# Optimization experiments

Measured on AMD Instinct MI355X. Metric: run time of the kernel, lower is better.

Reference implementation:

```python
import jax, jax.numpy as jnp
import numpy as np

B, T, D = 2, 512, 1024
H = 16
DH = D // H          # 64 head dim
E = 8                # experts
K = 2                # top-k routing
F = 4 * D            # expert hidden dim


def _layernorm(x, s, b, eps=1e-5):
    mu = jnp.mean(x, axis=-1, keepdims=True)
    var = jnp.var(x, axis=-1, keepdims=True)
    return (x - mu) * jax.lax.rsqrt(var + eps) * s + b


def setup_inputs() -> dict:
    key = jax.random.key(0)
    ks = jax.random.split(key, 16)
    sd = 0.02
    return {
        "x": jax.random.normal(ks[0], (B, T, D), jnp.float32),
        "text_state": jax.random.normal(ks[1], (B, D), jnp.float32),
        "ln1_s": jnp.ones((D,), jnp.float32),
        "ln1_b": jnp.zeros((D,), jnp.float32),
        "w_qkv": jax.random.normal(ks[2], (D, 3 * D), jnp.float32) * sd,
        "b_qkv": jnp.zeros((3 * D,), jnp.float32),
        "w_o": jax.random.normal(ks[3], (D, D), jnp.float32) * sd,
        "b_o": jnp.zeros((D,), jnp.float32),
        "rel_bias": jax.random.normal(ks[4], (H, 2 * T - 1), jnp.float32) * sd,
        "ln2_s": jnp.ones((D,), jnp.float32),
        "ln2_b": jnp.zeros((D,), jnp.float32),
        "w_txt": jax.random.normal(ks[5], (D, D), jnp.float32) * sd,
        "b_txt": jnp.zeros((D,), jnp.float32),
        "w_r": jax.random.normal(ks[6], (D, E), jnp.float32) * sd,
        "b_r": jnp.zeros((E,), jnp.float32),
        "w1": jax.random.normal(ks[7], (E, D, F), jnp.float32) * sd,
        "b1": jnp.zeros((E, F), jnp.float32),
        "w2": jax.random.normal(ks[8], (E, F, D), jnp.float32) * sd,
        "b2": jnp.zeros((E, D), jnp.float32),
    }


def reference(x, text_state, ln1_s, ln1_b, w_qkv, b_qkv, w_o, b_o, rel_bias,
              ln2_s, ln2_b, w_txt, b_txt, w_r, b_r, w1, b1, w2, b2):
    # ---- temporal-bias multi-head self-attention (pre-LN, residual) ----
    h = _layernorm(x, ln1_s, ln1_b)
    qkv = (h @ w_qkv + b_qkv).reshape(B, T, 3, H, DH)
    q, k, v = qkv[:, :, 0], qkv[:, :, 1], qkv[:, :, 2]       # [B,T,H,DH]
    scores = jnp.einsum("bthd,bshd->bhts", q, k) / np.sqrt(DH).astype(np.float32)
    idx = jnp.arange(T)
    rel = idx[None, :] - idx[:, None] + (T - 1)              # [T,T] in [0, 2T-2]
    scores = scores + rel_bias[:, rel][None]                 # broadcast [1,H,T,T]
    attn = jax.nn.softmax(scores, axis=-1)
    ctx = jnp.einsum("bhts,bshd->bthd", attn, v).reshape(B, T, D)
    x = x + ctx @ w_o + b_o

    # ---- top-k MoE feed-forward with text-conditioned router ----
    h2 = _layernorm(x, ln2_s, ln2_b)
    router_in = h2 + (text_state @ w_txt + b_txt)[:, None, :]
    probs = jax.nn.softmax(router_in @ w_r + b_r, axis=-1)   # [B,T,E]
    topv, topi = jax.lax.top_k(probs, K)                     # [B,T,K]
    gates = topv / jnp.sum(topv, axis=-1, keepdims=True)
    gates_full = jnp.einsum("btk,btke->bte", gates, jax.nn.one_hot(topi, E, dtype=x.dtype))
    # dense grouped-expert compute, sparsely combined (same math as dispatch)
    hid = jax.nn.gelu(jnp.einsum("btd,edf->btef", h2, w1) + b1)      # [B,T,E,F]
    eout = jnp.einsum("btef,efd->bted", hid, w2) + b2                # [B,T,E,D]
    y = jnp.einsum("bte,bted->btd", gates_full, eout)
    x = x + y

    diag = jnp.mean(probs, axis=(0, 1))                      # expert load [E]
    return x, diag
```

## Files before the change

kernel.cpp:

```cpp
#include <hip/hip_runtime.h>
#include <hip/hip_bf16.h>
#include <math.h>

#define BB 2
#define TT 512
#define DD 1024
#define HH 16
#define DHH 64
#define EE 8
#define FF 4096
#define NTOK 1024
#define CAP 2560

typedef __attribute__((ext_vector_type(4))) float f32x4;
typedef __attribute__((ext_vector_type(8))) short short8;

__device__ __forceinline__ short f2b(float f) {
    __hip_bfloat16 h = __float2bfloat16(f);
    return *reinterpret_cast<short*>(&h);
}

__device__ __forceinline__ void gload16(const short* g, short* l) {
    __builtin_amdgcn_global_load_lds((const __attribute__((address_space(1))) unsigned int*)g,
                                     (__attribute__((address_space(3))) unsigned int*)l,
                                     16, 0, 0);
}

template <int BF>
__global__ __launch_bounds__(256) void ln_kernel(const float* __restrict__ x,
                                                 const float* __restrict__ s,
                                                 const float* __restrict__ b,
                                                 void* __restrict__ outp) {
    int row = blockIdx.x;
    int tid = threadIdx.x;
    const float* xr = x + (size_t)row * DD;
    float sm = 0.f, sq = 0.f;
    for (int i = tid; i < DD; i += 256) {
        float v = xr[i];
        sm += v; sq += v * v;
    }
    #pragma unroll
    for (int o = 32; o; o >>= 1) {
        sm += __shfl_down(sm, o);
        sq += __shfl_down(sq, o);
    }
    __shared__ float r1[4], r2[4];
    if ((tid & 63) == 0) { r1[tid >> 6] = sm; r2[tid >> 6] = sq; }
    __syncthreads();
    float tot  = r1[0] + r1[1] + r1[2] + r1[3];
    float totq = r2[0] + r2[1] + r2[2] + r2[3];
    float mu  = tot * (1.f / DD);
    float var = totq * (1.f / DD) - mu * mu;
    float inv = rsqrtf(var + 1e-5f);
    for (int i = tid; i < DD; i += 256) {
        float v = (xr[i] - mu) * inv * s[i] + b[i];
        if (BF) ((short*)outp)[(size_t)row * DD + i] = f2b(v);
        else    ((float*)outp)[(size_t)row * DD + i] = v;
    }
}

__global__ __launch_bounds__(256) void transpose_cast(const float* __restrict__ src,
                                                      short* __restrict__ dst,
                                                      int K, int N) {
    __shared__ float t[32][33];
    src += (size_t)blockIdx.z * K * N;
    dst += (size_t)blockIdx.z * K * N;
    int k0 = blockIdx.y * 32, n0 = blockIdx.x * 32;
    int tx = threadIdx.x & 31, ty = threadIdx.x >> 5;
    #pragma unroll
    for (int p = 0; p < 4; p++) {
        int k = k0 + ty + p * 8;
        t[ty + p * 8][tx] = src[(size_t)k * N + n0 + tx];
    }
    __syncthreads();
    #pragma unroll
    for (int p = 0; p < 4; p++) {
        int n = n0 + ty + p * 8;
        dst[(size_t)n * K + k0 + tx] = f2b(t[tx][ty + p * 8]);
    }
}

__global__ __launch_bounds__(256) void v_transpose(const short* __restrict__ Vb,
                                                   short* __restrict__ VTb) {
    __shared__ short t[32][33];
    int bh = blockIdx.z;
    const short* src = Vb + (size_t)bh * TT * DHH;
    short* dst = VTb + (size_t)bh * DHH * TT;
    int t0 = blockIdx.x * 32, d0 = blockIdx.y * 32;
    int tx = threadIdx.x & 31, ty = threadIdx.x >> 5;
    #pragma unroll
    for (int p = 0; p < 4; p++)
        t[ty + p * 8][tx] = src[(size_t)(t0 + ty + p * 8) * DHH + d0 + tx];
    __syncthreads();
    #pragma unroll
    for (int p = 0; p < 4; p++)
        dst[(size_t)(d0 + ty + p * 8) * TT + t0 + tx] = t[tx][ty + p * 8];
}

__device__ __forceinline__ void gemm_loop(const short* __restrict__ A,
                                          const short* __restrict__ B,
                                          int K, short* As, short* Bs,
                                          f32x4 acc[2][2], int m0, int n0, int tid) {
    int wave = tid >> 6, lane = tid & 63;
    int wr = wave >> 1, wc = wave & 1;
    int lrow = lane & 15, lk = lane >> 4;
    int sr = tid >> 3, ss = tid & 7;
    int sswz = (ss ^ (sr & 7)) * 8;
    const short* Ag0 = A + (size_t)(m0 + sr) * K + sswz;
    const short* Ag1 = A + (size_t)(m0 + sr + 32) * K + sswz;
    const short* Bg0 = B + (size_t)(n0 + sr) * K + sswz;
    const short* Bg1 = B + (size_t)(n0 + sr + 32) * K + sswz;
    short* lA0 = As + wave * 512;
    short* lA1 = As + 2048 + wave * 512;
    short* lB0 = Bs + wave * 512;
    short* lB1 = Bs + 2048 + wave * 512;
    for (int k0 = 0; k0 < K; k0 += 64) {
        gload16(Ag0 + k0, lA0);
        gload16(Ag1 + k0, lA1);
        gload16(Bg0 + k0, lB0);
        gload16(Bg1 + k0, lB1);
        __syncthreads();
        #pragma unroll
        for (int kk = 0; kk < 2; kk++) {
            int slot = kk * 4 + lk;
            short8 a[2], b[2];
            #pragma unroll
            for (int i = 0; i < 2; i++) {
                int row = wr * 32 + i * 16 + lrow;
                uint4 v = ((const uint4*)As)[row * 8 + (slot ^ (row & 7))];
                a[i] = *(short8*)&v;
            }
            #pragma unroll
            for (int j = 0; j < 2; j++) {
                int row = wc * 32 + j * 16 + lrow;
                uint4 v = ((const uint4*)Bs)[row * 8 + (slot ^ (row & 7))];
                b[j] = *(short8*)&v;
            }
            #pragma unroll
            for (int i = 0; i < 2; i++)
                #pragma unroll
                for (int j = 0; j < 2; j++)
                    acc[i][j] = __builtin_amdgcn_mfma_f32_16x16x32_bf16(a[i], b[j], acc[i][j], 0, 0, 0);
        }
        __syncthreads();
    }
}

template <int MODE>
__global__ __launch_bounds__(256) void gemm_mfma(const short* __restrict__ A,
                                                 const short* __restrict__ Bw,
                                                 const float* __restrict__ bias,
                                                 const float* __restrict__ res,
                                                 float* __restrict__ C,
                                                 int N, int K) {
    __shared__ short As[4096];
    __shared__ short Bs[4096];
    int tid = threadIdx.x;
    int m0 = blockIdx.y * 64, n0 = blockIdx.x * 64;
    f32x4 acc[2][2] = {};
    gemm_loop(A, Bw, K, As, Bs, acc, m0, n0, tid);
    int wave = tid >> 6, lane = tid & 63;
    int wr = wave >> 1, wc = wave & 1;
    int lrow = lane & 15, lk = lane >> 4;
    #pragma unroll
    for (int i = 0; i < 2; i++) {
        #pragma unroll
        for (int j = 0; j < 2; j++) {
            int col = n0 + wc * 32 + j * 16 + lrow;
            float bv = bias[col];
            #pragma unroll
            for (int r = 0; r < 4; r++) {
                int row = m0 + wr * 32 + i * 16 + lk * 4 + r;
                float v = acc[i][j][r] + bv;
                if (MODE == 1) v += res[(size_t)row * N + col];
                C[(size_t)row * N + col] = v;
            }
        }
    }
}

__global__ __launch_bounds__(256) void qkv_mfma(const short* __restrict__ A,
                                                const short* __restrict__ Bw,
                                                const float* __restrict__ bias,
                                                short* __restrict__ Qb,
                                                short* __restrict__ Kb,
                                                short* __restrict__ Vb) {
    __shared__ short As[4096];
    __shared__ short Bs[4096];
    int tid = threadIdx.x;
    int m0 = blockIdx.y * 64, n0 = blockIdx.x * 64;
    f32x4 acc[2][2] = {};
    gemm_loop(A, Bw, DD, As, Bs, acc, m0, n0, tid);
    int wave = tid >> 6, lane = tid & 63;
    int wr = wave >> 1, wc = wave & 1;
    int lrow = lane & 15, lk = lane >> 4;
    int part = n0 >> 10;
    int h = (n0 & 1023) >> 6;
    short* dst = (part == 0) ? Qb : ((part == 1) ? Kb : Vb);
    #pragma unroll
    for (int i = 0; i < 2; i++) {
        #pragma unroll
        for (int j = 0; j < 2; j++) {
            int d = wc * 32 + j * 16 + lrow;
            float bv = bias[n0 + d];
            #pragma unroll
            for (int r = 0; r < 4; r++) {
                int row = m0 + wr * 32 + i * 16 + lk * 4 + r;
                int b = row >> 9, t = row & (TT - 1);
                dst[(((size_t)(b * HH + h)) * TT + t) * DHH + d] = f2b(acc[i][j][r] + bv);
            }
        }
    }
}

__global__ __launch_bounds__(256) void scores_mfma(const short* __restrict__ Qb,
                                                   const short* __restrict__ Kb,
                                                   float* __restrict__ S) {
    __shared__ short As[4096];
    __shared__ short Bs[4096];
    int tid = threadIdx.x;
    int bh = blockIdx.z;
    const short* A = Qb + (size_t)bh * TT * DHH;
    const short* B = Kb + (size_t)bh * TT * DHH;
    float* Sp = S + (size_t)bh * TT * TT;
    int m0 = blockIdx.y * 64, n0 = blockIdx.x * 64;
    f32x4 acc[2][2] = {};
    gemm_loop(A, B, DHH, As, Bs, acc, m0, n0, tid);
    int wave = tid >> 6, lane = tid & 63;
    int wr = wave >> 1, wc = wave & 1;
    int lrow = lane & 15, lk = lane >> 4;
    #pragma unroll
    for (int i = 0; i < 2; i++)
        #pragma unroll
        for (int j = 0; j < 2; j++) {
            int col = n0 + wc * 32 + j * 16 + lrow;
            #pragma unroll
            for (int r = 0; r < 4; r++) {
                int row = m0 + wr * 32 + i * 16 + lk * 4 + r;
                Sp[(size_t)row * TT + col] = acc[i][j][r];
            }
        }
}

__global__ __launch_bounds__(256) void softmax_kernel(const float* __restrict__ S,
                                                      const float* __restrict__ rel_bias,
                                                      short* __restrict__ P) {
    int row = blockIdx.x * 4 + (threadIdx.x >> 6);
    int lane = threadIdx.x & 63;
    int t = row & (TT - 1), h = (row >> 9) & (HH - 1);
    const float* Sr = S + (size_t)row * TT;
    const float* br = rel_bias + h * (2 * TT - 1) + (TT - 1) - t;
    float v[8];
    float mx = -1e30f;
    #pragma unroll
    for (int i = 0; i < 8; i++) {
        int s = lane + i * 64;
        v[i] = Sr[s] * 0.125f + br[s];
        mx = fmaxf(mx, v[i]);
    }
    #pragma unroll
    for (int o = 32; o; o >>= 1) mx = fmaxf(mx, __shfl_xor(mx, o));
    float sum = 0.f;
    #pragma unroll
    for (int i = 0; i < 8; i++) { v[i] = expf(v[i] - mx); sum += v[i]; }
    #pragma unroll
    for (int o = 32; o; o >>= 1) sum += __shfl_xor(sum, o);
    float inv = 1.f / sum;
    #pragma unroll
    for (int i = 0; i < 8; i++)
        P[(size_t)row * TT + lane + i * 64] = f2b(v[i] * inv);
}

__global__ __launch_bounds__(256) void pv_mfma(const short* __restrict__ P,
                                               const short* __restrict__ VTb,
                                               short* __restrict__ ctxb) {
    __shared__ short As[4096];
    __shared__ short Bs[4096];
    int tid = threadIdx.x;
    int bh = blockIdx.z;
    int h = bh & (HH - 1), b = bh >> 4;
    const short* A = P + (size_t)bh * TT * TT;
    const short* B = VTb + (size_t)bh * DHH * TT;
    int m0 = blockIdx.y * 64;
    f32x4 acc[2][2] = {};
    gemm_loop(A, B, TT, As, Bs, acc, m0, 0, tid);
    int wave = tid >> 6, lane = tid & 63;
    int wr = wave >> 1, wc = wave & 1;
    int lrow = lane & 15, lk = lane >> 4;
    #pragma unroll
    for (int i = 0; i < 2; i++)
        #pragma unroll
        for (int j = 0; j < 2; j++) {
            int d = wc * 32 + j * 16 + lrow;
            #pragma unroll
            for (int r = 0; r < 4; r++) {
                int row = m0 + wr * 32 + i * 16 + lk * 4 + r;
                ctxb[((size_t)(b * TT + row)) * DD + h * DHH + d] = f2b(acc[i][j][r]);
            }
        }
}

__global__ __launch_bounds__(256) void moe_gemm1_mfma(const short* __restrict__ Ag,
                                                      const short* __restrict__ W1t,
                                                      const float* __restrict__ b1,
                                                      const int* __restrict__ counts,
                                                      const int* __restrict__ offs,
                                                      short* __restrict__ hid) {
    int e = blockIdx.y >> 4, tile = blockIdx.y & 15;
    int cnt = counts[e];
    int pcnt = (cnt + 63) & ~63;
    int row0 = tile * 64;
    if (row0 >= pcnt) return;
    int base = offs[e];
    const short* A  = Ag + (size_t)base * DD;
    const short* Bw = W1t + (size_t)e * FF * DD;
    __shared__ short As[4096];
    __shared__ short Bs[4096];
    int tid = threadIdx.x;
    int n0 = blockIdx.x * 64;
    f32x4 acc[2][2] = {};
    gemm_loop(A, Bw, DD, As, Bs, acc, row0, n0, tid);
    int wave = tid >> 6, lane = tid & 63;
    int wr = wave >> 1, wc = wave & 1;
    int lrow = lane & 15, lk = lane >> 4;
    #pragma unroll
    for (int i = 0; i < 2; i++) {
        #pragma unroll
        for (int j = 0; j < 2; j++) {
            int col = n0 + wc * 32 + j * 16 + lrow;
            float bv = b1[e * FF + col];
            #pragma unroll
            for (int r = 0; r < 4; r++) {
                int row = row0 + wr * 32 + i * 16 + lk * 4 + r;
                float v = acc[i][j][r] + bv;
                float u = 0.7978845608028654f * (v + 0.044715f * v * v * v);
                float g = 0.5f * v * (1.f + tanhf(u));
                hid[(size_t)(base + row) * FF + col] = f2b(g);
            }
        }
    }
}

__global__ __launch_bounds__(256) void moe_gemm2_mfma(const short* __restrict__ hid,
                                                      const short* __restrict__ W2t,
                                                      const float* __restrict__ b2,
                                                      const float* __restrict__ pair_gate,
                                                      const int* __restrict__ counts,
                                                      const int* __restrict__ offs,
                                                      float* __restrict__ pair_out) {
    int e = blockIdx.y >> 4, tile = blockIdx.y & 15;
    int cnt = counts[e];
    int pcnt = (cnt + 63) & ~63;
    int row0 = tile * 64;
    if (row0 >= pcnt) return;
    int base = offs[e];
    const short* A  = hid + (size_t)base * FF;
    const short* Bw = W2t + (size_t)e * DD * FF;
    __shared__ short As[4096];
    __shared__ short Bs[4096];
    int tid = threadIdx.x;
    int n0 = blockIdx.x * 64;
    f32x4 acc[2][2] = {};
    gemm_loop(A, Bw, FF, As, Bs, acc, row0, n0, tid);
    int wave = tid >> 6, lane = tid & 63;
    int wr = wave >> 1, wc = wave & 1;
    int lrow = lane & 15, lk = lane >> 4;
    #pragma unroll
    for (int i = 0; i < 2; i++) {
        #pragma unroll
        for (int j = 0; j < 2; j++) {
            int col = n0 + wc * 32 + j * 16 + lrow;
            float bv = b2[e * DD + col];
            #pragma unroll
            for (int r = 0; r < 4; r++) {
                int row = row0 + wr * 32 + i * 16 + lk * 4 + r;
                float g = pair_gate[base + row];
                pair_out[(size_t)(base + row) * DD + col] = g * (acc[i][j][r] + bv);
            }
        }
    }
}

__global__ __launch_bounds__(256) void txt_kernel(const float* __restrict__ ts,
                                                  const float* __restrict__ w,
                                                  const float* __restrict__ bias,
                                                  float* __restrict__ out) {
    int gid = blockIdx.x * 256 + threadIdx.x;
    int b = gid >> 10;
    int n = gid & (DD - 1);
    float acc = 0.f;
    for (int d = 0; d < DD; d++) acc += ts[b * DD + d] * w[(size_t)d * DD + n];
    out[gid] = acc + bias[n];
}

__global__ __launch_bounds__(256) void router_kernel(const float* __restrict__ h2,
                                                     const float* __restrict__ txt,
                                                     const float* __restrict__ w_r,
                                                     const float* __restrict__ b_r,
                                                     float* __restrict__ probs,
                                                     float* __restrict__ gates,
                                                     int* __restrict__ counts) {
    int row = blockIdx.x;
    int b = row >> 9;
    int tid = threadIdx.x;
    float acc[EE] = {};
    for (int d = tid; d < DD; d += 256) {
        float r = h2[(size_t)row * DD + d] + txt[b * DD + d];
        #pragma unroll
        for (int e = 0; e < EE; e++) acc[e] += r * w_r[d * EE + e];
    }
    #pragma unroll
    for (int e = 0; e < EE; e++)
        #pragma unroll
        for (int o = 32; o; o >>= 1) acc[e] += __shfl_down(acc[e], o);
    __shared__ float lds[4][EE];
    int lane = tid & 63, w = tid >> 6;
    if (lane == 0)
        for (int e = 0; e < EE; e++) lds[w][e] = acc[e];
    __syncthreads();
    if (tid == 0) {
        float lg[EE], p[EE];
        float mx = -1e30f;
        for (int e = 0; e < EE; e++) {
            lg[e] = lds[0][e] + lds[1][e] + lds[2][e] + lds[3][e] + b_r[e];
            mx = fmaxf(mx, lg[e]);
        }
        float sum = 0.f;
        for (int e = 0; e < EE; e++) { p[e] = expf(lg[e] - mx); sum += p[e]; }
        float invs = 1.f / sum;
        for (int e = 0; e < EE; e++) { p[e] *= invs; probs[row * EE + e] = p[e]; }
        int i1 = 0;
        for (int e = 1; e < EE; e++) if (p[e] > p[i1]) i1 = e;
        int i2 = (i1 == 0) ? 1 : 0;
        for (int e = 0; e < EE; e++) if (e != i1 && p[e] > p[i2]) i2 = e;
        float gs = p[i1] + p[i2];
        for (int e = 0; e < EE; e++) gates[row * EE + e] = 0.f;
        gates[row * EE + i1] = p[i1] / gs;
        gates[row * EE + i2] = p[i2] / gs;
        atomicAdd(&counts[i1], 1);
        atomicAdd(&counts[i2], 1);
    }
}

__global__ void offs_kernel(const int* __restrict__ counts, int* __restrict__ offs) {
    if (threadIdx.x == 0) {
        int acc = 0;
        for (int e = 0; e < EE; e++) { offs[e] = acc; acc += (counts[e] + 63) & ~63; }
    }
}

__global__ __launch_bounds__(256) void scatter_kernel(const float* __restrict__ gates,
                                                      const int* __restrict__ offs,
                                                      int* __restrict__ fill,
                                                      int* __restrict__ tok_pos,
                                                      float* __restrict__ pair_gate) {
    int t = blockIdx.x * 256 + threadIdx.x;
    if (t >= NTOK) return;
    int slot = 0;
    for (int e = 0; e < EE; e++) {
        float g = gates[t * EE + e];
        if (g > 0.f) {
            int pos = offs[e] + atomicAdd(&fill[e], 1);
            tok_pos[t * 2 + slot] = pos;
            pair_gate[pos] = g;
            slot++;
        }
    }
}

__global__ __launch_bounds__(256) void gather_tokens(const float* __restrict__ h2,
                                                     const int* __restrict__ tok_pos,
                                                     short* __restrict__ Ag) {
    int i = blockIdx.x;
    int pos = tok_pos[i];
    int t = i >> 1;
    int d = threadIdx.x * 4;
    #pragma unroll
    for (int k = 0; k < 4; k++)
        Ag[(size_t)pos * DD + d + k] = f2b(h2[(size_t)t * DD + d + k]);
}

__global__ __launch_bounds__(256) void diag_kernel(const float* __restrict__ probs,
                                                   float* __restrict__ out) {
    int e = blockIdx.x;
    int tid = threadIdx.x;
    float s = 0.f;
    for (int t = tid; t < NTOK; t += 256) s += probs[t * EE + e];
    #pragma unroll
    for (int o = 32; o; o >>= 1) s += __shfl_down(s, o);
    __shared__ float red[4];
    if ((tid & 63) == 0) red[tid >> 6] = s;
    __syncthreads();
    if (tid == 0) out[e] = (red[0] + red[1] + red[2] + red[3]) * (1.f / NTOK);
}

__global__ __launch_bounds__(256) void finaladd_kernel(float* __restrict__ out,
                                                       const float* __restrict__ pair_out,
                                                       const int* __restrict__ tok_pos) {
    int t = blockIdx.x;
    int pA = tok_pos[2 * t], pB = tok_pos[2 * t + 1];
    int d = threadIdx.x * 4;
    float4 a = *(const float4*)&out[(size_t)t * DD + d];
    float4 u = *(const float4*)&pair_out[(size_t)pA * DD + d];
    float4 v = *(const float4*)&pair_out[(size_t)pB * DD + d];
    a.x += u.x + v.x; a.y += u.y + v.y; a.z += u.z + v.z; a.w += u.w + v.w;
    *(float4*)&out[(size_t)t * DD + d] = a;
}

extern "C" void kernel_launch(void* const* d_in, const int* in_sizes, int n_in,
                              void* d_out, int out_size, void* d_ws, size_t ws_size,
                              hipStream_t stream) {
    const float* x          = (const float*)d_in[0];
    const float* text_state = (const float*)d_in[1];
    const float* ln1_s      = (const float*)d_in[2];
    const float* ln1_b      = (const float*)d_in[3];
    const float* w_qkv      = (const float*)d_in[4];
    const float* b_qkv      = (const float*)d_in[5];
    const float* w_o        = (const float*)d_in[6];
    const float* b_o        = (const float*)d_in[7];
    const float* rel_bias   = (const float*)d_in[8];
    const float* ln2_s      = (const float*)d_in[9];
    const float* ln2_b      = (const float*)d_in[10];
    const float* w_txt      = (const float*)d_in[11];
    const float* b_txt      = (const float*)d_in[12];
    const float* w_r        = (const float*)d_in[13];
    const float* b_r        = (const float*)d_in[14];
    const float* w1         = (const float*)d_in[15];
    const float* b1         = (const float*)d_in[16];
    const float* w2         = (const float*)d_in[17];
    const float* b2         = (const float*)d_in[18];

    float* out = (float*)d_out;

    char* p = (char*)d_ws;
    auto alloc = [&](size_t bytes) { char* r = p; p += (bytes + 255) & ~(size_t)255; return r; };
    short* h1b      = (short*)alloc((size_t)NTOK * DD * 2);
    short* Qb       = (short*)alloc((size_t)NTOK * DD * 2);
    short* Kb       = (short*)alloc((size_t)NTOK * DD * 2);
    short* Vb       = (short*)alloc((size_t)NTOK * DD * 2);
    short* VTb      = (short*)alloc((size_t)NTOK * DD * 2);
    char*  region1  = alloc((size_t)BB * HH * TT * TT * 4);
    char*  region2  = alloc((size_t)BB * HH * TT * TT * 2);
    short* ctxb     = (short*)alloc((size_t)NTOK * DD * 2);
    float* h2       = (float*)alloc((size_t)NTOK * DD * 4);
    float* txt      = (float*)alloc((size_t)BB * DD * 4);
    float* probs    = (float*)alloc((size_t)NTOK * EE * 4);
    float* gates    = (float*)alloc((size_t)NTOK * EE * 4);
    float* pair_gate= (float*)alloc((size_t)CAP * 4);
    int*   counts   = (int*)alloc(8 * 4);
    int*   fill     = (int*)alloc(8 * 4);
    int*   offs     = (int*)alloc(8 * 4);
    int*   tok_pos  = (int*)alloc((size_t)NTOK * 2 * 4);
    short* wqkvT    = (short*)alloc((size_t)3 * DD * DD * 2);
    short* woT      = (short*)alloc((size_t)DD * DD * 2);
    short* w1T      = (short*)alloc((size_t)EE * FF * DD * 2);
    short* w2T      = (short*)alloc((size_t)EE * DD * FF * 2);

    float* S        = (float*)region1;
    short* P        = (short*)region2;
    short* Ag       = (short*)region1;
    short* hid      = (short*)(region1 + ((size_t)CAP * DD * 2 + 255 & ~(size_t)255));
    float* pair_out = (float*)region2;

    transpose_cast<<<dim3(3 * DD / 32, DD / 32, 1), 256, 0, stream>>>(w_qkv, wqkvT, DD, 3 * DD);
    transpose_cast<<<dim3(DD / 32, DD / 32, 1), 256, 0, stream>>>(w_o, woT, DD, DD);
    transpose_cast<<<dim3(FF / 32, DD / 32, EE), 256, 0, stream>>>(w1, w1T, DD, FF);
    transpose_cast<<<dim3(DD / 32, FF / 32, EE), 256, 0, stream>>>(w2, w2T, FF, DD);

    ln_kernel<1><<<NTOK, 256, 0, stream>>>(x, ln1_s, ln1_b, h1b);
    qkv_mfma<<<dim3(3 * DD / 64, NTOK / 64), 256, 0, stream>>>(h1b, wqkvT, b_qkv, Qb, Kb, Vb);
    v_transpose<<<dim3(TT / 32, DHH / 32, BB * HH), 256, 0, stream>>>(Vb, VTb);
    scores_mfma<<<dim3(TT / 64, TT / 64, BB * HH), 256, 0, stream>>>(Qb, Kb, S);
    softmax_kernel<<<BB * HH * TT / 4, 256, 0, stream>>>(S, rel_bias, P);
    pv_mfma<<<dim3(1, TT / 64, BB * HH), 256, 0, stream>>>(P, VTb, ctxb);
    gemm_mfma<1><<<dim3(DD / 64, NTOK / 64), 256, 0, stream>>>(ctxb, woT, b_o, x, out, DD, DD);
    ln_kernel<0><<<NTOK, 256, 0, stream>>>(out, ln2_s, ln2_b, h2);
    txt_kernel<<<(BB * DD) / 256, 256, 0, stream>>>(text_state, w_txt, b_txt, txt);
    hipMemsetAsync(counts, 0, 8 * 4, stream);
    hipMemsetAsync(fill, 0, 8 * 4, stream);
    hipMemsetAsync(Ag, 0, (size_t)CAP * DD * 2, stream);
    router_kernel<<<NTOK, 256, 0, stream>>>(h2, txt, w_r, b_r, probs, gates, counts);
    offs_kernel<<<1, 64, 0, stream>>>(counts, offs);
    scatter_kernel<<<NTOK / 256, 256, 0, stream>>>(gates, offs, fill, tok_pos, pair_gate);
    gather_tokens<<<NTOK * 2, 256, 0, stream>>>(h2, tok_pos, Ag);
    diag_kernel<<<EE, 256, 0, stream>>>(probs, out + (size_t)NTOK * DD);
    moe_gemm1_mfma<<<dim3(FF / 64, EE * 16), 256, 0, stream>>>(Ag, w1T, b1, counts, offs, hid);
    moe_gemm2_mfma<<<dim3(DD / 64, EE * 16), 256, 0, stream>>>(hid, w2T, b2, pair_gate, counts, offs, pair_out);
    finaladd_kernel<<<NTOK, 256, 0, stream>>>(out, pair_out, tok_pos);
}
```

Measured before the change: 415.2 us.

## Widen MFMA GEMM tiles to 64x128 and vectorize the weight transpose-cast

Adds a wider GEMM main loop in which each block computes a 64x128 output tile. Each wave now holds 2x4 MFMA accumulators, so A-tile reuse doubles and the number of blocks halves. The QKV, scores, output-projection and both MoE GEMMs use it; the PV GEMM keeps the 64-wide loop. The weight transpose-cast moves to 64x64 tiles with float4 loads and short4 stores to cut memory transactions. The MoE grid also doubles its per-expert tile slots, which adds blocks that exit early, and the larger LDS and register footprint may lower occupancy.

```diff
diff --git a/kernel.cpp b/kernel.cpp
--- a/kernel.cpp
+++ b/kernel.cpp
@@ -62,21 +62,28 @@
 __global__ __launch_bounds__(256) void transpose_cast(const float* __restrict__ src,
                                                       short* __restrict__ dst,
                                                       int K, int N) {
-    __shared__ float t[32][33];
+    __shared__ float t[64][65];
     src += (size_t)blockIdx.z * K * N;
     dst += (size_t)blockIdx.z * K * N;
-    int k0 = blockIdx.y * 32, n0 = blockIdx.x * 32;
-    int tx = threadIdx.x & 31, ty = threadIdx.x >> 5;
+    int k0 = blockIdx.y * 64, n0 = blockIdx.x * 64;
+    int rr = threadIdx.x >> 4;
+    int cc = (threadIdx.x & 15) * 4;
     #pragma unroll
     for (int p = 0; p < 4; p++) {
-        int k = k0 + ty + p * 8;
-        t[ty + p * 8][tx] = src[(size_t)k * N + n0 + tx];
+        float4 v = *(const float4*)&src[(size_t)(k0 + rr + p * 16) * N + n0 + cc];
+        t[rr + p * 16][cc]     = v.x;
+        t[rr + p * 16][cc + 1] = v.y;
+        t[rr + p * 16][cc + 2] = v.z;
+        t[rr + p * 16][cc + 3] = v.w;
     }
     __syncthreads();
     #pragma unroll
     for (int p = 0; p < 4; p++) {
-        int n = n0 + ty + p * 8;
-        dst[(size_t)n * K + k0 + tx] = f2b(t[tx][ty + p * 8]);
+        int n = rr + p * 16;
+        short4 o;
+        o.x = f2b(t[cc][n]); o.y = f2b(t[cc + 1][n]);
+        o.z = f2b(t[cc + 2][n]); o.w = f2b(t[cc + 3][n]);
+        *(short4*)&dst[(size_t)(n0 + n) * K + k0 + cc] = o;
     }
 }
 
@@ -97,10 +104,65 @@
         dst[(size_t)(d0 + ty + p * 8) * TT + t0 + tx] = t[tx][ty + p * 8];
 }
 
-__device__ __forceinline__ void gemm_loop(const short* __restrict__ A,
-                                          const short* __restrict__ B,
-                                          int K, short* As, short* Bs,
-                                          f32x4 acc[2][2], int m0, int n0, int tid) {
+__device__ __forceinline__ void gemm_loop_w(const short* __restrict__ A,
+                                            const short* __restrict__ B,
+                                            int K, short* As, short* Bs,
+                                            f32x4 acc[2][4], int m0, int n0, int tid) {
+    int wave = tid >> 6, lane = tid & 63;
+    int wr = wave >> 1, wc = wave & 1;
+    int lrow = lane & 15, lk = lane >> 4;
+    int sr = tid >> 3, ss = tid & 7;
+    int sswz = (ss ^ (sr & 7)) * 8;
+    const short* Ag0 = A + (size_t)(m0 + sr) * K + sswz;
+    const short* Ag1 = A + (size_t)(m0 + sr + 32) * K + sswz;
+    const short* Bg0 = B + (size_t)(n0 + sr) * K + sswz;
+    const short* Bg1 = B + (size_t)(n0 + sr + 32) * K + sswz;
+    const short* Bg2 = B + (size_t)(n0 + sr + 64) * K + sswz;
+    const short* Bg3 = B + (size_t)(n0 + sr + 96) * K + sswz;
+    short* lA0 = As + wave * 512;
+    short* lA1 = As + 2048 + wave * 512;
+    short* lB0 = Bs + wave * 512;
+    short* lB1 = Bs + 2048 + wave * 512;
+    short* lB2 = Bs + 4096 + wave * 512;
+    short* lB3 = Bs + 6144 + wave * 512;
+    for (int k0 = 0; k0 < K; k0 += 64) {
+        gload16(Ag0 + k0, lA0);
+        gload16(Ag1 + k0, lA1);
+        gload16(Bg0 + k0, lB0);
+        gload16(Bg1 + k0, lB1);
+        gload16(Bg2 + k0, lB2);
+        gload16(Bg3 + k0, lB3);
+        __syncthreads();
+        #pragma unroll
+        for (int kk = 0; kk < 2; kk++) {
+            int slot = kk * 4 + lk;
+            short8 a[2], b[4];
+            #pragma unroll
+            for (int i = 0; i < 2; i++) {
+                int row = wr * 32 + i * 16 + lrow;
+                uint4 v = ((const uint4*)As)[row * 8 + (slot ^ (row & 7))];
+                a[i] = *(short8*)&v;
+            }
+            #pragma unroll
+            for (int j = 0; j < 4; j++) {
+                int row = wc * 64 + j * 16 + lrow;
+                uint4 v = ((const uint4*)Bs)[row * 8 + (slot ^ (row & 7))];
+                b[j] = *(short8*)&v;
+            }
+            #pragma unroll
+            for (int i = 0; i < 2; i++)
+                #pragma unroll
+                for (int j = 0; j < 4; j++)
+                    acc[i][j] = __builtin_amdgcn_mfma_f32_16x16x32_bf16(a[i], b[j], acc[i][j], 0, 0, 0);
+        }
+        __syncthreads();
+    }
+}
+
+__device__ __forceinline__ void gemm_loop64(const short* __restrict__ A,
+                                            const short* __restrict__ B,
+                                            int K, short* As, short* Bs,
+                                            f32x4 acc[2][2], int m0, int n0, int tid) {
     int wave = tid >> 6, lane = tid & 63;
     int wr = wave >> 1, wc = wave & 1;
     int lrow = lane & 15, lk = lane >> 4;
@@ -154,19 +216,19 @@
                                                  float* __restrict__ C,
                                                  int N, int K) {
     __shared__ short As[4096];
-    __shared__ short Bs[4096];
-    int tid = threadIdx.x;
-    int m0 = blockIdx.y * 64, n0 = blockIdx.x * 64;
-    f32x4 acc[2][2] = {};
-    gemm_loop(A, Bw, K, As, Bs, acc, m0, n0, tid);
+    __shared__ short Bs[8192];
+    int tid = threadIdx.x;
+    int m0 = blockIdx.y * 64, n0 = blockIdx.x * 128;
+    f32x4 acc[2][4] = {};
+    gemm_loop_w(A, Bw, K, As, Bs, acc, m0, n0, tid);
     int wave = tid >> 6, lane = tid & 63;
     int wr = wave >> 1, wc = wave & 1;
     int lrow = lane & 15, lk = lane >> 4;
     #pragma unroll
     for (int i = 0; i < 2; i++) {
         #pragma unroll
-        for (int j = 0; j < 2; j++) {
-            int col = n0 + wc * 32 + j * 16 + lrow;
+        for (int j = 0; j < 4; j++) {
+            int col = n0 + wc * 64 + j * 16 + lrow;
             float bv = bias[col];
             #pragma unroll
             for (int r = 0; r < 4; r++) {
@@ -186,23 +248,24 @@
                                                 short* __restrict__ Kb,
                                                 short* __restrict__ Vb) {
     __shared__ short As[4096];
-    __shared__ short Bs[4096];
-    int tid = threadIdx.x;
-    int m0 = blockIdx.y * 64, n0 = blockIdx.x * 64;
-    f32x4 acc[2][2] = {};
-    gemm_loop(A, Bw, DD, As, Bs, acc, m0, n0, tid);
-    int wave = tid >> 6, lane = tid & 63;
-    int wr = wave >> 1, wc = wave & 1;
-    int lrow = lane & 15, lk = lane >> 4;
-    int part = n0 >> 10;
-    int h = (n0 & 1023) >> 6;
-    short* dst = (part == 0) ? Qb : ((part == 1) ? Kb : Vb);
+    __shared__ short Bs[8192];
+    int tid = threadIdx.x;
+    int m0 = blockIdx.y * 64, n0 = blockIdx.x * 128;
+    f32x4 acc[2][4] = {};
+    gemm_loop_w(A, Bw, DD, As, Bs, acc, m0, n0, tid);
+    int wave = tid >> 6, lane = tid & 63;
+    int wr = wave >> 1, wc = wave & 1;
+    int lrow = lane & 15, lk = lane >> 4;
     #pragma unroll
     for (int i = 0; i < 2; i++) {
         #pragma unroll
-        for (int j = 0; j < 2; j++) {
-            int d = wc * 32 + j * 16 + lrow;
-            float bv = bias[n0 + d];
+        for (int j = 0; j < 4; j++) {
+            int col = n0 + wc * 64 + j * 16 + lrow;
+            int part = col >> 10;
+            int rem = col & 1023;
+            int h = rem >> 6, d = rem & 63;
+            short* dst = (part == 0) ? Qb : ((part == 1) ? Kb : Vb);
+            float bv = bias[col];
             #pragma unroll
             for (int r = 0; r < 4; r++) {
                 int row = m0 + wr * 32 + i * 16 + lk * 4 + r;
@@ -217,23 +280,23 @@
                                                    const short* __restrict__ Kb,
                                                    float* __restrict__ S) {
     __shared__ short As[4096];
-    __shared__ short Bs[4096];
+    __shared__ short Bs[8192];
     int tid = threadIdx.x;
     int bh = blockIdx.z;
     const short* A = Qb + (size_t)bh * TT * DHH;
     const short* B = Kb + (size_t)bh * TT * DHH;
     float* Sp = S + (size_t)bh * TT * TT;
-    int m0 = blockIdx.y * 64, n0 = blockIdx.x * 64;
-    f32x4 acc[2][2] = {};
-    gemm_loop(A, B, DHH, As, Bs, acc, m0, n0, tid);
+    int m0 = blockIdx.y * 64, n0 = blockIdx.x * 128;
+    f32x4 acc[2][4] = {};
+    gemm_loop_w(A, B, DHH, As, Bs, acc, m0, n0, tid);
     int wave = tid >> 6, lane = tid & 63;
     int wr = wave >> 1, wc = wave & 1;
     int lrow = lane & 15, lk = lane >> 4;
     #pragma unroll
     for (int i = 0; i < 2; i++)
         #pragma unroll
-        for (int j = 0; j < 2; j++) {
-            int col = n0 + wc * 32 + j * 16 + lrow;
+        for (int j = 0; j < 4; j++) {
+            int col = n0 + wc * 64 + j * 16 + lrow;
             #pragma unroll
             for (int r = 0; r < 4; r++) {
                 int row = m0 + wr * 32 + i * 16 + lk * 4 + r;
@@ -283,7 +346,7 @@
     const short* B = VTb + (size_t)bh * DHH * TT;
     int m0 = blockIdx.y * 64;
     f32x4 acc[2][2] = {};
-    gemm_loop(A, B, TT, As, Bs, acc, m0, 0, tid);
+    gemm_loop64(A, B, TT, As, Bs, acc, m0, 0, tid);
     int wave = tid >> 6, lane = tid & 63;
     int wr = wave >> 1, wc = wave & 1;
     int lrow = lane & 15, lk = lane >> 4;
@@ -306,7 +369,7 @@
                                                       const int* __restrict__ counts,
                                                       const int* __restrict__ offs,
                                                       short* __restrict__ hid) {
-    int e = blockIdx.y >> 4, tile = blockIdx.y & 15;
+    int e = blockIdx.y >> 5, tile = blockIdx.y & 31;
     int cnt = counts[e];
     int pcnt = (cnt + 63) & ~63;
     int row0 = tile * 64;
@@ -315,19 +378,19 @@
     const short* A  = Ag + (size_t)base * DD;
     const short* Bw = W1t + (size_t)e * FF * DD;
     __shared__ short As[4096];
-    __shared__ short Bs[4096];
-    int tid = threadIdx.x;
-    int n0 = blockIdx.x * 64;
-    f32x4 acc[2][2] = {};
-    gemm_loop(A, Bw, DD, As, Bs, acc, row0, n0, tid);
+    __shared__ short Bs[8192];
+    int tid = threadIdx.x;
+    int n0 = blockIdx.x * 128;
+    f32x4 acc[2][4] = {};
+    gemm_loop_w(A, Bw, DD, As, Bs, acc, row0, n0, tid);
     int wave = tid >> 6, lane = tid & 63;
     int wr = wave >> 1, wc = wave & 1;
     int lrow = lane & 15, lk = lane >> 4;
     #pragma unroll
     for (int i = 0; i < 2; i++) {
         #pragma unroll
-        for (int j = 0; j < 2; j++) {
-            int col = n0 + wc * 32 + j * 16 + lrow;
+        for (int j = 0; j < 4; j++) {
+            int col = n0 + wc * 64 + j * 16 + lrow;
             float bv = b1[e * FF + col];
             #pragma unroll
             for (int r = 0; r < 4; r++) {
@@ -348,7 +411,7 @@
                                                       const int* __restrict__ counts,
                                                       const int* __restrict__ offs,
                                                       float* __restrict__ pair_out) {
-    int e = blockIdx.y >> 4, tile = blockIdx.y & 15;
+    int e = blockIdx.y >> 5, tile = blockIdx.y & 31;
     int cnt = counts[e];
     int pcnt = (cnt + 63) & ~63;
     int row0 = tile * 64;
@@ -357,19 +420,19 @@
     const short* A  = hid + (size_t)base * FF;
     const short* Bw = W2t + (size_t)e * DD * FF;
     __shared__ short As[4096];
-    __shared__ short Bs[4096];
-    int tid = threadIdx.x;
-    int n0 = blockIdx.x * 64;
-    f32x4 acc[2][2] = {};
-    gemm_loop(A, Bw, FF, As, Bs, acc, row0, n0, tid);
+    __shared__ short Bs[8192];
+    int tid = threadIdx.x;
+    int n0 = blockIdx.x * 128;
+    f32x4 acc[2][4] = {};
+    gemm_loop_w(A, Bw, FF, As, Bs, acc, row0, n0, tid);
     int wave = tid >> 6, lane = tid & 63;
     int wr = wave >> 1, wc = wave & 1;
     int lrow = lane & 15, lk = lane >> 4;
     #pragma unroll
     for (int i = 0; i < 2; i++) {
         #pragma unroll
-        for (int j = 0; j < 2; j++) {
-            int col = n0 + wc * 32 + j * 16 + lrow;
+        for (int j = 0; j < 4; j++) {
+            int col = n0 + wc * 64 + j * 16 + lrow;
             float bv = b2[e * DD + col];
             #pragma unroll
             for (int r = 0; r < 4; r++) {
@@ -562,18 +625,18 @@
     short* hid      = (short*)(region1 + ((size_t)CAP * DD * 2 + 255 & ~(size_t)255));
     float* pair_out = (float*)region2;
 
-    transpose_cast<<<dim3(3 * DD / 32, DD / 32, 1), 256, 0, stream>>>(w_qkv, wqkvT, DD, 3 * DD);
-    transpose_cast<<<dim3(DD / 32, DD / 32, 1), 256, 0, stream>>>(w_o, woT, DD, DD);
-    transpose_cast<<<dim3(FF / 32, DD / 32, EE), 256, 0, stream>>>(w1, w1T, DD, FF);
-    transpose_cast<<<dim3(DD / 32, FF / 32, EE), 256, 0, stream>>>(w2, w2T, FF, DD);
+    transpose_cast<<<dim3(3 * DD / 64, DD / 64, 1), 256, 0, stream>>>(w_qkv, wqkvT, DD, 3 * DD);
+    transpose_cast<<<dim3(DD / 64, DD / 64, 1), 256, 0, stream>>>(w_o, woT, DD, DD);
+    transpose_cast<<<dim3(FF / 64, DD / 64, EE), 256, 0, stream>>>(w1, w1T, DD, FF);
+    transpose_cast<<<dim3(DD / 64, FF / 64, EE), 256, 0, stream>>>(w2, w2T, FF, DD);
 
     ln_kernel<1><<<NTOK, 256, 0, stream>>>(x, ln1_s, ln1_b, h1b);
-    qkv_mfma<<<dim3(3 * DD / 64, NTOK / 64), 256, 0, stream>>>(h1b, wqkvT, b_qkv, Qb, Kb, Vb);
+    qkv_mfma<<<dim3(3 * DD / 128, NTOK / 64), 256, 0, stream>>>(h1b, wqkvT, b_qkv, Qb, Kb, Vb);
     v_transpose<<<dim3(TT / 32, DHH / 32, BB * HH), 256, 0, stream>>>(Vb, VTb);
-    scores_mfma<<<dim3(TT / 64, TT / 64, BB * HH), 256, 0, stream>>>(Qb, Kb, S);
+    scores_mfma<<<dim3(TT / 128, TT / 64, BB * HH), 256, 0, stream>>>(Qb, Kb, S);
     softmax_kernel<<<BB * HH * TT / 4, 256, 0, stream>>>(S, rel_bias, P);
     pv_mfma<<<dim3(1, TT / 64, BB * HH), 256, 0, stream>>>(P, VTb, ctxb);
-    gemm_mfma<1><<<dim3(DD / 64, NTOK / 64), 256, 0, stream>>>(ctxb, woT, b_o, x, out, DD, DD);
+    gemm_mfma<1><<<dim3(DD / 128, NTOK / 64), 256, 0, stream>>>(ctxb, woT, b_o, x, out, DD, DD);
     ln_kernel<0><<<NTOK, 256, 0, stream>>>(out, ln2_s, ln2_b, h2);
     txt_kernel<<<(BB * DD) / 256, 256, 0, stream>>>(text_state, w_txt, b_txt, txt);
     hipMemsetAsync(counts, 0, 8 * 4, stream);
@@ -584,7 +647,7 @@
     scatter_kernel<<<NTOK / 256, 256, 0, stream>>>(gates, offs, fill, tok_pos, pair_gate);
     gather_tokens<<<NTOK * 2, 256, 0, stream>>>(h2, tok_pos, Ag);
     diag_kernel<<<EE, 256, 0, stream>>>(probs, out + (size_t)NTOK * DD);
-    moe_gemm1_mfma<<<dim3(FF / 64, EE * 16), 256, 0, stream>>>(Ag, w1T, b1, counts, offs, hid);
-    moe_gemm2_mfma<<<dim3(DD / 64, EE * 16), 256, 0, stream>>>(hid, w2T, b2, pair_gate, counts, offs, pair_out);
+    moe_gemm1_mfma<<<dim3(FF / 128, EE * 32), 256, 0, stream>>>(Ag, w1T, b1, counts, offs, hid);
+    moe_gemm2_mfma<<<dim3(DD / 128, EE * 32), 256, 0, stream>>>(hid, w2T, b2, pair_gate, counts, offs, pair_out);
     finaladd_kernel<<<NTOK, 256, 0, stream>>>(out, pair_out, tok_pos);
 }
```

After: 437.0 us. +5.3%, slower.
